# Performance work log

Hardware: AMD Instinct MI355X
Metric: run time of the kernel (lower is better)

## Reference

```python
import jax, jax.numpy as jnp
import numpy as np

N = 65536
DIM = 128
MARKET = 32
STYLE = 32
E = 9          # num_market_experts
TOP_K = 3
ALPHA = 1e-4


def setup_inputs() -> dict:
    key = jax.random.key(0)
    ks = jax.random.split(key, 8)
    sc = lambda k, shape, s: (jax.random.normal(k, shape, jnp.float32) * s)
    return {
        "x": jax.random.normal(ks[0], (N, 1, DIM), jnp.float32),
        # Wr: Linear(dim -> market_dim)
        "Wr_w": sc(ks[1], (DIM, MARKET), 0.05),
        "Wr_b": jnp.zeros((MARKET,), jnp.float32),
        # Wl: Linear(N -> 1), applied over the N axis
        "Wl_w": sc(ks[2], (N,), 0.005),
        "Wl_b": jnp.zeros((1,), jnp.float32),
        # router: Linear(dim + market_dim -> E)
        "router_w": sc(ks[3], (DIM + MARKET, E), 0.05),
        "router_b": jnp.zeros((E,), jnp.float32),
        # experts: style params + 2-layer MLP (dim+style -> dim -> dim)
        "styles": sc(ks[4], (E, STYLE), 1.0),
        "W1": sc(ks[5], (E, DIM + STYLE, DIM), 0.05),
        "b1": jnp.zeros((E, DIM), jnp.float32),
        "W2": sc(ks[6], (E, DIM, DIM), 0.05),
        "b2": jnp.zeros((E, DIM), jnp.float32),
    }


def reference(x, Wr_w, Wr_b, Wl_w, Wl_b, router_w, router_b, styles, W1, b1, W2, b2):
    n, s, d = x.shape  # [N, 1, dim]

    # market summary: Wr (relu MLP, dropout=identity in eval), then Wl over N axis
    market = jax.nn.relu(x @ Wr_w + Wr_b)                       # [N,1,M]
    market_g = jnp.einsum('nsm,n->sm', market, Wl_w) + Wl_b     # [1,M]
    market_exp = jnp.broadcast_to(market_g[None], (n, s, market.shape[-1]))
    x_market = jnp.concatenate([x, market_exp], axis=-1)        # [N,1,dim+M]

    # noisy-topk router (noisy=False)
    logits = x_market @ router_w + router_b                     # [N,1,E]
    _top_vals, top_idx = jax.lax.top_k(logits, TOP_K)           # [N,1,K]
    mask = (jax.nn.one_hot(top_idx, E) > 0).any(axis=-2)        # [N,1,E] bool
    sparse = jnp.where(mask, logits, -jnp.inf)
    gating = jax.nn.softmax(sparse, axis=-1)                    # [N,1,E], zeros off top-k

    # sequence-wise auxiliary load-balancing loss
    T = n * s
    flat_g = gating.reshape(-1, E)
    fi = mask.reshape(-1, E).sum(axis=0).astype(jnp.float32) * (E / (TOP_K * T))
    Pi = flat_g.mean(axis=0)
    aux_loss = ALPHA * jnp.sum(fi * Pi)

    # expert MLPs: dense-masked combine (gating is exactly 0 for unselected experts,
    # so this equals the original gather/scatter dispatch)
    flat_x = x.reshape(-1, d)                                   # [T,d]
    W1x = W1[:, :d, :]                                          # [E,d,h]
    W1s = W1[:, d:, :]                                          # [E,style,h]
    style_bias = jnp.einsum('es,esh->eh', styles, W1s) + b1     # [E,h]
    h = jax.nn.relu(jnp.einsum('nd,edh->neh', flat_x, W1x) + style_bias[None])
    out_e = jnp.einsum('neh,ehd->ned', h, W2) + b2[None]        # [T,E,d]
    out = jnp.einsum('ne,ned->nd', flat_g, out_e)               # [T,d]

    return out.reshape(n, s, d), aux_loss
```

## Files before the change

kernel.cpp:

```cpp
#include <hip/hip_runtime.h>
#include <hip/hip_bf16.h>
#include <math.h>

#define NTOK 65536
#define DIM  128
#define NE   9
#define TOPK 3
#define ALPHA_C 1e-4f

using bf16x8 = __attribute__((ext_vector_type(8))) short;
using f32x4  = __attribute__((ext_vector_type(4))) float;

static constexpr size_t OFF_MG   = 0;
static constexpr size_t OFF_CNT  = 128;
static constexpr size_t OFF_GSUM = 192;
static constexpr size_t OFF_SB   = 256;
static constexpr size_t OFF_W1F  = 4864;
static constexpr size_t OFF_W2F  = 299776;

__device__ __forceinline__ unsigned short f2bf(float f) {
    __hip_bfloat16 h = __float2bfloat16(f);
    return *reinterpret_cast<unsigned short*>(&h);
}

__global__ __launch_bounds__(256) void k_market(const float* __restrict__ x,
    const float* __restrict__ Wrw, const float* __restrict__ Wrb,
    const float* __restrict__ Wlw, float* __restrict__ mg_acc)
{
    __shared__ float xs[64 * 132];
    __shared__ float wr[128 * 32];
    __shared__ float part[256][8];
    int tid = threadIdx.x;
    int base = blockIdx.x * 64;

    const float4* x4 = (const float4*)x + (size_t)base * 32;
    for (int i = tid; i < 64 * 32; i += 256) {
        int row = i >> 5, c4 = i & 31;
        *(float4*)(&xs[row * 132 + c4 * 4]) = x4[i];
    }
    const float4* w4 = (const float4*)Wrw;
    float4* wr4 = (float4*)wr;
    for (int i = tid; i < 128 * 32 / 4; i += 256) wr4[i] = w4[i];
    __syncthreads();

    int tok = tid >> 2, sub = tid & 3, m0 = sub * 8;
    float acc[8];
    #pragma unroll
    for (int k = 0; k < 8; ++k) acc[k] = 0.f;
    for (int d = 0; d < 128; ++d) {
        float xv = xs[tok * 132 + d];
        #pragma unroll
        for (int k = 0; k < 8; ++k) acc[k] += xv * wr[d * 32 + m0 + k];
    }
    float wl = Wlw[base + tok];
    #pragma unroll
    for (int k = 0; k < 8; ++k) {
        float v = acc[k] + Wrb[m0 + k];
        part[tid][k] = (v > 0.f ? v : 0.f) * wl;
    }
    __syncthreads();
    if (tid < 32) {
        int m = tid;
        float s = 0.f;
        for (int t = 0; t < 64; ++t) s += part[t * 4 + (m >> 3)][m & 7];
        atomicAdd(&mg_acc[m], s);
    }
}

__global__ __launch_bounds__(256) void k_prepw(const float* __restrict__ W1,
    const float* __restrict__ W2, unsigned short* __restrict__ W1F,
    unsigned short* __restrict__ W2F)
{
    int e = blockIdx.x;
    int n = blockIdx.y;
    int tid = threadIdx.x;
    int kk = tid >> 6, l = tid & 63;
    int row0 = kk * 32 + (l >> 4) * 8;
    int col  = n * 16 + (l & 15);
    const float* W1e = W1 + (size_t)e * 20480;
    const float* W2e = W2 + (size_t)e * 16384;
    size_t ob = (size_t)e * 16384 + n * 2048 + kk * 512 + l * 8;
    unsigned short u1[8], u2[8];
    #pragma unroll
    for (int j = 0; j < 8; ++j) {
        u1[j] = f2bf(W1e[(size_t)(row0 + j) * 128 + col]);
        u2[j] = f2bf(W2e[(size_t)(row0 + j) * 128 + col]);
    }
    *(ushort4*)(W1F + ob)     = *(ushort4*)(u1);
    *(ushort4*)(W1F + ob + 4) = *(ushort4*)(u1 + 4);
    *(ushort4*)(W2F + ob)     = *(ushort4*)(u2);
    *(ushort4*)(W2F + ob + 4) = *(ushort4*)(u2 + 4);
}

__global__ void k_stylebias(const float* __restrict__ styles, const float* __restrict__ W1,
                            const float* __restrict__ b1, float* __restrict__ sb)
{
    int e = blockIdx.x, h = threadIdx.x;
    float acc = b1[e * 128 + h];
    for (int s = 0; s < 32; ++s)
        acc += styles[e * 32 + s] * W1[(size_t)e * 20480 + (size_t)(128 + s) * 128 + h];
    sb[e * 128 + h] = acc;
}

__global__ void k_aux(const unsigned* __restrict__ cnt, const float* __restrict__ gsum,
                      float* __restrict__ out)
{
    float a = 0.f;
    for (int e = 0; e < 9; ++e) {
        float fi = (float)cnt[e] * ((float)NE / ((float)TOPK * (float)NTOK));
        float Pi = gsum[e] / (float)NTOK;
        a += fi * Pi;
    }
    out[(size_t)NTOK * DIM] = ALPHA_C * a;
}

__global__ __launch_bounds__(256) void k_fused(const float* __restrict__ x,
    const float* __restrict__ rweights, const float* __restrict__ rb,
    const float* __restrict__ mg, const float* __restrict__ Wlb,
    const unsigned short* __restrict__ W1F, const unsigned short* __restrict__ W2F,
    const float* __restrict__ sbg, const float* __restrict__ b2g,
    unsigned* __restrict__ cnt, float* __restrict__ gsum,
    float* __restrict__ out)
{
    __shared__ unsigned short xs[64 * 128];
    __shared__ unsigned short hs[2][64 * 128];
    __shared__ float garr[64][12];
    __shared__ float ce[9];
    __shared__ unsigned lcount[9];
    __shared__ float lgsum[9];

    float* part = (float*)hs;
    float* rwp  = (float*)hs + 2304;

    int tid = threadIdx.x;
    int base = blockIdx.x * 64;

    for (int i = tid; i < 160 * 9; i += 256) rwp[i] = rweights[i];
    if (tid < 9) { lcount[tid] = 0u; lgsum[tid] = 0.f; }
    __syncthreads();

    int tok = tid >> 2, sub = tid & 3;
    {
        float acc[9];
        #pragma unroll
        for (int e = 0; e < 9; ++e) acc[e] = 0.f;
        const float* xrow = x + (size_t)(base + tok) * 128 + sub * 32;
        for (int d = 0; d < 32; ++d) {
            float xv = xrow[d];
            #pragma unroll
            for (int e = 0; e < 9; ++e) acc[e] += xv * rwp[(sub * 32 + d) * 9 + e];
        }
        #pragma unroll
        for (int e = 0; e < 9; ++e) part[(tok * 4 + sub) * 9 + e] = acc[e];
    }
    if (tid < 9) {
        float c = rb[tid];
        float wlb = Wlb[0];
        for (int m = 0; m < 32; ++m) c += (mg[m] + wlb) * rwp[(128 + m) * 9 + tid];
        ce[tid] = c;
    }
    {
        const float4* x4 = (const float4*)x;
        for (int i = tid; i < 64 * 32; i += 256) {
            int row = i >> 5, p = i & 31;
            float4 v = x4[(size_t)(base + row) * 32 + p];
            unsigned short u[4] = { f2bf(v.x), f2bf(v.y), f2bf(v.z), f2bf(v.w) };
            int sw = ((((p >> 1) ^ (row & 7)) << 4) | ((p & 1) << 3));
            *(ushort4*)((char*)xs + row * 256 + sw) = *(ushort4*)u;
        }
    }
    __syncthreads();

    if (sub == 0) {
        float lg[9];
        #pragma unroll
        for (int e = 0; e < 9; ++e)
            lg[e] = ce[e] + part[(tok * 4 + 0) * 9 + e] + part[(tok * 4 + 1) * 9 + e]
                  + part[(tok * 4 + 2) * 9 + e] + part[(tok * 4 + 3) * 9 + e];
        int used = 0;
        int bi[3]; float bv[3];
        for (int k = 0; k < 3; ++k) {
            float best = -1e30f; int b = -1;
            for (int e = 0; e < 9; ++e)
                if (!((used >> e) & 1) && lg[e] > best) { best = lg[e]; b = e; }
            bi[k] = b; bv[k] = best; used |= 1 << b;
        }
        float p3[3]; float s = 0.f;
        for (int k = 0; k < 3; ++k) { p3[k] = expf(bv[k] - bv[0]); s += p3[k]; }
        #pragma unroll
        for (int e = 0; e < 12; ++e) garr[tok][e] = 0.f;
        for (int k = 0; k < 3; ++k) {
            float g = p3[k] / s;
            garr[tok][bi[k]] = g;
            atomicAdd(&lcount[bi[k]], 1u);
            atomicAdd(&lgsum[bi[k]], g);
        }
    }
    __syncthreads();
    if (tid < 9) {
        atomicAdd(&cnt[tid], lcount[tid]);
        atomicAdd(&gsum[tid], lgsum[tid]);
    }

    int lane = tid & 63, w = tid >> 6;
    int tl = lane & 15;
    int hq = lane >> 4;
    int xr = tl & 7;

    f32x4 acc_out[2][4];
    #pragma unroll
    for (int mi = 0; mi < 2; ++mi)
        #pragma unroll
        for (int ni = 0; ni < 4; ++ni) acc_out[mi][ni] = (f32x4){0.f, 0.f, 0.f, 0.f};

    #pragma unroll 1
    for (int e = 0; e < 9; ++e) {
        const unsigned short* A1 = W1F + (size_t)e * 16384 + (w * 2) * 2048 + lane * 8;
        const unsigned short* A2 = W2F + (size_t)e * 16384 + (w * 2) * 2048 + lane * 8;
        unsigned short* cur = hs[e & 1];

        bf16x8 a1[2][4];
        #pragma unroll
        for (int mi = 0; mi < 2; ++mi)
            #pragma unroll
            for (int kk = 0; kk < 4; ++kk)
                a1[mi][kk] = *(const bf16x8*)(A1 + mi * 2048 + kk * 512);

        float4 sbv0 = *(const float4*)(sbg + e * 128 + (w * 2 + 0) * 16 + hq * 4);
        float4 sbv1 = *(const float4*)(sbg + e * 128 + (w * 2 + 1) * 16 + hq * 4);
        f32x4 acc1[2][4];
        #pragma unroll
        for (int ni = 0; ni < 4; ++ni) {
            acc1[0][ni] = (f32x4){sbv0.x, sbv0.y, sbv0.z, sbv0.w};
            acc1[1][ni] = (f32x4){sbv1.x, sbv1.y, sbv1.z, sbv1.w};
        }

        #pragma unroll
        for (int kk = 0; kk < 4; ++kk) {
            #pragma unroll
            for (int ni = 0; ni < 4; ++ni) {
                bf16x8 b = *(const bf16x8*)((const char*)xs + (ni * 16 + tl) * 256
                               + ((((kk * 4 + hq) ^ xr) << 4)));
                acc1[0][ni] = __builtin_amdgcn_mfma_f32_16x16x32_bf16(a1[0][kk], b, acc1[0][ni], 0, 0, 0);
                acc1[1][ni] = __builtin_amdgcn_mfma_f32_16x16x32_bf16(a1[1][kk], b, acc1[1][ni], 0, 0, 0);
            }
        }

        bf16x8 a2[2][4];
        #pragma unroll
        for (int mi = 0; mi < 2; ++mi)
            #pragma unroll
            for (int kk = 0; kk < 4; ++kk)
                a2[mi][kk] = *(const bf16x8*)(A2 + mi * 2048 + kk * 512);

        #pragma unroll
        for (int ni = 0; ni < 4; ++ni) {
            int t = ni * 16 + tl;
            float g = garr[t][e];
            char* rowp = (char*)cur + t * 256;
            #pragma unroll
            for (int mi = 0; mi < 2; ++mi) {
                f32x4 v = acc1[mi][ni];
                unsigned short u[4];
                u[0] = f2bf(fmaxf(v[0], 0.f) * g);
                u[1] = f2bf(fmaxf(v[1], 0.f) * g);
                u[2] = f2bf(fmaxf(v[2], 0.f) * g);
                u[3] = f2bf(fmaxf(v[3], 0.f) * g);
                int chunk = (w * 2 + mi) * 2 + (hq >> 1);
                int off = (hq & 1) * 8;
                *(ushort4*)(rowp + (((chunk ^ xr) << 4) | off)) = *(ushort4*)u;
            }
        }
        __syncthreads();

        #pragma unroll
        for (int kk = 0; kk < 4; ++kk) {
            #pragma unroll
            for (int ni = 0; ni < 4; ++ni) {
                bf16x8 b = *(const bf16x8*)((const char*)cur + (ni * 16 + tl) * 256
                               + ((((kk * 4 + hq) ^ xr) << 4)));
                acc_out[0][ni] = __builtin_amdgcn_mfma_f32_16x16x32_bf16(a2[0][kk], b, acc_out[0][ni], 0, 0, 0);
                acc_out[1][ni] = __builtin_amdgcn_mfma_f32_16x16x32_bf16(a2[1][kk], b, acc_out[1][ni], 0, 0, 0);
            }
        }
    }

    #pragma unroll
    for (int mi = 0; mi < 2; ++mi) {
        int d0 = (w * 2 + mi) * 16 + hq * 4;
        float4 b2v[9];
        #pragma unroll
        for (int e = 0; e < 9; ++e) b2v[e] = *(const float4*)(b2g + e * 128 + d0);
        #pragma unroll
        for (int ni = 0; ni < 4; ++ni) {
            int t = ni * 16 + tl;
            float4 bias = {0.f, 0.f, 0.f, 0.f};
            #pragma unroll
            for (int e = 0; e < 9; ++e) {
                float g = garr[t][e];
                bias.x += g * b2v[e].x; bias.y += g * b2v[e].y;
                bias.z += g * b2v[e].z; bias.w += g * b2v[e].w;
            }
            f32x4 v = acc_out[mi][ni];
            float4 r = {v[0] + bias.x, v[1] + bias.y, v[2] + bias.z, v[3] + bias.w};
            *(float4*)(out + (size_t)(base + t) * 128 + d0) = r;
        }
    }
}

extern "C" void kernel_launch(void* const* d_in, const int* in_sizes, int n_in,
                              void* d_out, int out_size, void* d_ws, size_t ws_size,
                              hipStream_t stream) {
    const float* x      = (const float*)d_in[0];
    const float* Wrw    = (const float*)d_in[1];
    const float* Wrb    = (const float*)d_in[2];
    const float* Wlw    = (const float*)d_in[3];
    const float* Wlb    = (const float*)d_in[4];
    const float* rw     = (const float*)d_in[5];
    const float* rb     = (const float*)d_in[6];
    const float* styles = (const float*)d_in[7];
    const float* W1     = (const float*)d_in[8];
    const float* b1     = (const float*)d_in[9];
    const float* W2     = (const float*)d_in[10];
    const float* b2     = (const float*)d_in[11];
    float* out = (float*)d_out;

    char* ws = (char*)d_ws;
    float*          mg    = (float*)(ws + OFF_MG);
    unsigned*       cnt   = (unsigned*)(ws + OFF_CNT);
    float*          gsum  = (float*)(ws + OFF_GSUM);
    float*          sbp   = (float*)(ws + OFF_SB);
    unsigned short* W1F   = (unsigned short*)(ws + OFF_W1F);
    unsigned short* W2F   = (unsigned short*)(ws + OFF_W2F);

    hipMemsetAsync(ws, 0, 256, stream);

    k_market<<<1024, 256, 0, stream>>>(x, Wrw, Wrb, Wlw, mg);
    k_prepw<<<dim3(9, 8), 256, 0, stream>>>(W1, W2, W1F, W2F);
    k_stylebias<<<9, 128, 0, stream>>>(styles, W1, b1, sbp);
    k_fused<<<1024, 256, 0, stream>>>(x, rw, rb, mg, Wlb, W1F, W2F, sbp, b2,
                                      cnt, gsum, out);
    k_aux<<<1, 1, 0, stream>>>(cnt, gsum, out);
}
```

Measured before the change: 199.3 us.

## Merge prep kernels into one launch, single-buffer hidden LDS, tweak reductions

Combines the market summary, weight conversion and style-bias kernels into one launch whose roles are picked by block index, cutting launch overhead and letting those stages run concurrently. The market reduction now uses wave shuffles and a per-wave partial array instead of a shared-memory scan. In the fused kernel the hidden buffer is single-buffered, which halves that LDS use and may raise occupancy, at the cost of an extra barrier per expert. The router dot product switches to an interleaved x access pattern, changing how each thread reads x and the router weights.

```diff
diff --git a/kernel.cpp b/kernel.cpp
--- a/kernel.cpp
+++ b/kernel.cpp
@@ -23,83 +23,94 @@
     return *reinterpret_cast<unsigned short*>(&h);
 }
 
-__global__ __launch_bounds__(256) void k_market(const float* __restrict__ x,
+__global__ __launch_bounds__(256) void k_prep(const float* __restrict__ x,
     const float* __restrict__ Wrw, const float* __restrict__ Wrb,
-    const float* __restrict__ Wlw, float* __restrict__ mg_acc)
+    const float* __restrict__ Wlw, float* __restrict__ mg_acc,
+    const float* __restrict__ W1, const float* __restrict__ W2,
+    unsigned short* __restrict__ W1F, unsigned short* __restrict__ W2F,
+    const float* __restrict__ styles, const float* __restrict__ b1,
+    float* __restrict__ sb)
 {
-    __shared__ float xs[64 * 132];
-    __shared__ float wr[128 * 32];
-    __shared__ float part[256][8];
+    __shared__ float smem[64 * 132 + 128 * 32];
+    __shared__ float wpart[4][32];
+    int bid = blockIdx.x;
     int tid = threadIdx.x;
-    int base = blockIdx.x * 64;
-
-    const float4* x4 = (const float4*)x + (size_t)base * 32;
-    for (int i = tid; i < 64 * 32; i += 256) {
-        int row = i >> 5, c4 = i & 31;
-        *(float4*)(&xs[row * 132 + c4 * 4]) = x4[i];
-    }
-    const float4* w4 = (const float4*)Wrw;
-    float4* wr4 = (float4*)wr;
-    for (int i = tid; i < 128 * 32 / 4; i += 256) wr4[i] = w4[i];
-    __syncthreads();
-
-    int tok = tid >> 2, sub = tid & 3, m0 = sub * 8;
-    float acc[8];
-    #pragma unroll
-    for (int k = 0; k < 8; ++k) acc[k] = 0.f;
-    for (int d = 0; d < 128; ++d) {
-        float xv = xs[tok * 132 + d];
-        #pragma unroll
-        for (int k = 0; k < 8; ++k) acc[k] += xv * wr[d * 32 + m0 + k];
-    }
-    float wl = Wlw[base + tok];
-    #pragma unroll
-    for (int k = 0; k < 8; ++k) {
-        float v = acc[k] + Wrb[m0 + k];
-        part[tid][k] = (v > 0.f ? v : 0.f) * wl;
-    }
-    __syncthreads();
-    if (tid < 32) {
-        int m = tid;
-        float s = 0.f;
-        for (int t = 0; t < 64; ++t) s += part[t * 4 + (m >> 3)][m & 7];
-        atomicAdd(&mg_acc[m], s);
-    }
-}
-
-__global__ __launch_bounds__(256) void k_prepw(const float* __restrict__ W1,
-    const float* __restrict__ W2, unsigned short* __restrict__ W1F,
-    unsigned short* __restrict__ W2F)
-{
-    int e = blockIdx.x;
-    int n = blockIdx.y;
-    int tid = threadIdx.x;
-    int kk = tid >> 6, l = tid & 63;
-    int row0 = kk * 32 + (l >> 4) * 8;
-    int col  = n * 16 + (l & 15);
-    const float* W1e = W1 + (size_t)e * 20480;
-    const float* W2e = W2 + (size_t)e * 16384;
-    size_t ob = (size_t)e * 16384 + n * 2048 + kk * 512 + l * 8;
-    unsigned short u1[8], u2[8];
-    #pragma unroll
-    for (int j = 0; j < 8; ++j) {
-        u1[j] = f2bf(W1e[(size_t)(row0 + j) * 128 + col]);
-        u2[j] = f2bf(W2e[(size_t)(row0 + j) * 128 + col]);
-    }
-    *(ushort4*)(W1F + ob)     = *(ushort4*)(u1);
-    *(ushort4*)(W1F + ob + 4) = *(ushort4*)(u1 + 4);
-    *(ushort4*)(W2F + ob)     = *(ushort4*)(u2);
-    *(ushort4*)(W2F + ob + 4) = *(ushort4*)(u2 + 4);
-}
-
-__global__ void k_stylebias(const float* __restrict__ styles, const float* __restrict__ W1,
-                            const float* __restrict__ b1, float* __restrict__ sb)
-{
-    int e = blockIdx.x, h = threadIdx.x;
-    float acc = b1[e * 128 + h];
-    for (int s = 0; s < 32; ++s)
-        acc += styles[e * 32 + s] * W1[(size_t)e * 20480 + (size_t)(128 + s) * 128 + h];
-    sb[e * 128 + h] = acc;
+
+    if (bid < 1024) {
+        float* xs = smem;
+        float* wr = smem + 64 * 132;
+        int base = bid * 64;
+        const float4* x4g = (const float4*)x + (size_t)base * 32;
+        for (int i = tid; i < 2048; i += 256) {
+            int row = i >> 5, c = i & 31;
+            *(float4*)(xs + row * 132 + c * 4) = x4g[i];
+        }
+        for (int i = tid; i < 1024; i += 256)
+            ((float4*)wr)[i] = ((const float4*)Wrw)[i];
+        __syncthreads();
+
+        int lane = tid & 63, wv = tid >> 6;
+        int tok = wv * 16 + (lane >> 2), sub = lane & 3, m0 = sub * 8;
+        float acc[8];
+        #pragma unroll
+        for (int k = 0; k < 8; ++k) acc[k] = 0.f;
+        for (int c = 0; c < 32; ++c) {
+            float4 xv = *(const float4*)(xs + tok * 132 + c * 4);
+            float xa[4] = {xv.x, xv.y, xv.z, xv.w};
+            #pragma unroll
+            for (int dd = 0; dd < 4; ++dd)
+                #pragma unroll
+                for (int k = 0; k < 8; ++k)
+                    acc[k] += xa[dd] * wr[(c * 4 + dd) * 32 + m0 + k];
+        }
+        float wl = Wlw[base + tok];
+        #pragma unroll
+        for (int k = 0; k < 8; ++k) {
+            float v = acc[k] + Wrb[m0 + k];
+            acc[k] = (v > 0.f ? v : 0.f) * wl;
+        }
+        #pragma unroll
+        for (int off = 4; off <= 32; off <<= 1)
+            #pragma unroll
+            for (int k = 0; k < 8; ++k)
+                acc[k] += __shfl_xor(acc[k], off);
+        if (lane < 4)
+            #pragma unroll
+            for (int k = 0; k < 8; ++k) wpart[wv][lane * 8 + k] = acc[k];
+        __syncthreads();
+        if (tid < 32) {
+            float s = wpart[0][tid] + wpart[1][tid] + wpart[2][tid] + wpart[3][tid];
+            atomicAdd(&mg_acc[tid], s);
+        }
+    } else if (bid < 1096) {
+        int b = bid - 1024;
+        int e = b >> 3, n = b & 7;
+        int kk = tid >> 6, l = tid & 63;
+        int row0 = kk * 32 + (l >> 4) * 8;
+        int col  = n * 16 + (l & 15);
+        const float* W1e = W1 + (size_t)e * 20480;
+        const float* W2e = W2 + (size_t)e * 16384;
+        size_t ob = (size_t)e * 16384 + n * 2048 + kk * 512 + l * 8;
+        unsigned short u1[8], u2[8];
+        #pragma unroll
+        for (int j = 0; j < 8; ++j) {
+            u1[j] = f2bf(W1e[(size_t)(row0 + j) * 128 + col]);
+            u2[j] = f2bf(W2e[(size_t)(row0 + j) * 128 + col]);
+        }
+        *(ushort4*)(W1F + ob)     = *(ushort4*)(u1);
+        *(ushort4*)(W1F + ob + 4) = *(ushort4*)(u1 + 4);
+        *(ushort4*)(W2F + ob)     = *(ushort4*)(u2);
+        *(ushort4*)(W2F + ob + 4) = *(ushort4*)(u2 + 4);
+    } else {
+        int e = bid - 1096;
+        if (tid < 128) {
+            int h = tid;
+            float acc = b1[e * 128 + h];
+            for (int s = 0; s < 32; ++s)
+                acc += styles[e * 32 + s] * W1[(size_t)e * 20480 + (size_t)(128 + s) * 128 + h];
+            sb[e * 128 + h] = acc;
+        }
+    }
 }
 
 __global__ void k_aux(const unsigned* __restrict__ cnt, const float* __restrict__ gsum,
@@ -123,7 +134,7 @@
     float* __restrict__ out)
 {
     __shared__ unsigned short xs[64 * 128];
-    __shared__ unsigned short hs[2][64 * 128];
+    __shared__ unsigned short hs[64 * 128];
     __shared__ float garr[64][12];
     __shared__ float ce[9];
     __shared__ unsigned lcount[9];
@@ -144,11 +155,11 @@
         float acc[9];
         #pragma unroll
         for (int e = 0; e < 9; ++e) acc[e] = 0.f;
-        const float* xrow = x + (size_t)(base + tok) * 128 + sub * 32;
+        const float* xrow = x + (size_t)(base + tok) * 128 + sub;
         for (int d = 0; d < 32; ++d) {
-            float xv = xrow[d];
-            #pragma unroll
-            for (int e = 0; e < 9; ++e) acc[e] += xv * rwp[(sub * 32 + d) * 9 + e];
+            float xv = xrow[d * 4];
+            #pragma unroll
+            for (int e = 0; e < 9; ++e) acc[e] += xv * rwp[(d * 4 + sub) * 9 + e];
         }
         #pragma unroll
         for (int e = 0; e < 9; ++e) part[(tok * 4 + sub) * 9 + e] = acc[e];
@@ -217,7 +228,6 @@
     for (int e = 0; e < 9; ++e) {
         const unsigned short* A1 = W1F + (size_t)e * 16384 + (w * 2) * 2048 + lane * 8;
         const unsigned short* A2 = W2F + (size_t)e * 16384 + (w * 2) * 2048 + lane * 8;
-        unsigned short* cur = hs[e & 1];
 
         bf16x8 a1[2][4];
         #pragma unroll
@@ -257,7 +267,7 @@
         for (int ni = 0; ni < 4; ++ni) {
             int t = ni * 16 + tl;
             float g = garr[t][e];
-            char* rowp = (char*)cur + t * 256;
+            char* rowp = (char*)hs + t * 256;
             #pragma unroll
             for (int mi = 0; mi < 2; ++mi) {
                 f32x4 v = acc1[mi][ni];
@@ -277,12 +287,13 @@
         for (int kk = 0; kk < 4; ++kk) {
             #pragma unroll
             for (int ni = 0; ni < 4; ++ni) {
-                bf16x8 b = *(const bf16x8*)((const char*)cur + (ni * 16 + tl) * 256
+                bf16x8 b = *(const bf16x8*)((const char*)hs + (ni * 16 + tl) * 256
                                + ((((kk * 4 + hq) ^ xr) << 4)));
                 acc_out[0][ni] = __builtin_amdgcn_mfma_f32_16x16x32_bf16(a2[0][kk], b, acc_out[0][ni], 0, 0, 0);
                 acc_out[1][ni] = __builtin_amdgcn_mfma_f32_16x16x32_bf16(a2[1][kk], b, acc_out[1][ni], 0, 0, 0);
             }
         }
+        if (e != 8) __syncthreads();
     }
 
     #pragma unroll
@@ -335,9 +346,8 @@
 
     hipMemsetAsync(ws, 0, 256, stream);
 
-    k_market<<<1024, 256, 0, stream>>>(x, Wrw, Wrb, Wlw, mg);
-    k_prepw<<<dim3(9, 8), 256, 0, stream>>>(W1, W2, W1F, W2F);
-    k_stylebias<<<9, 128, 0, stream>>>(styles, W1, b1, sbp);
+    k_prep<<<1105, 256, 0, stream>>>(x, Wrw, Wrb, Wlw, mg, W1, W2, W1F, W2F,
+                                     styles, b1, sbp);
     k_fused<<<1024, 256, 0, stream>>>(x, rw, rb, mg, Wlb, W1F, W2F, sbp, b2,
                                       cnt, gsum, out);
     k_aux<<<1, 1, 0, stream>>>(cnt, gsum, out);
```

Measured after the change: 190.9 us. -4.2%, faster.
